# Performance work log

Hardware: AMD Instinct MI355X
Metric: run time of the kernel (lower is better)

The kernel has to match this reference:

```python
import jax, jax.numpy as jnp
import numpy as np
from jax import lax

P = 5
N_RATES = 8
N_SUB = 10
RATE_LO, RATE_HI = 0.01, 3.0
HJ_LO, HJ_HI = 0.0, 3.0


def gamma(x, lo, hi):
    return lo + (hi - lo) * jax.nn.sigmoid(x)


def chain_rhs(y, rates):
    # y: (B,5) [A,D,G,J,M]; rates: (B,8) [kf1..kf4, kr1..kr4]
    A, D, G, J, M = (y[..., i] for i in range(5))
    kf1, kf2, kf3, kf4, kr1, kr2, kr3, kr4 = (rates[..., i] for i in range(8))
    dA = -kf1 * A + kr1 * D
    dD = kf1 * A - kr1 * D - kf2 * D + kr2 * G
    dG = kf2 * D - kr2 * G - kf3 * G + kr3 * J
    dJ = kf3 * G - kr3 * J - kf4 * J + kr4 * M
    dM = kf4 * J - kr4 * M
    return jnp.stack([dA, dD, dG, dJ, dM], axis=-1)


def rk4_step(y, dt, rates):
    # dt: (B,1)
    k1 = chain_rhs(y, rates)
    k2 = chain_rhs(y + 0.5 * dt * k1, rates)
    k3 = chain_rhs(y + 0.5 * dt * k2, rates)
    k4 = chain_rhs(y + dt * k3, rates)
    y_next = y + dt / 6.0 * (k1 + 2.0 * k2 + 2.0 * k3 + k4)
    return jnp.maximum(y_next, 0.0)


def xavier(key, shape):
    fan_in, fan_out = shape[1], shape[0]
    lim = float(np.sqrt(6.0 / (fan_in + fan_out)))
    return jax.random.uniform(key, shape, jnp.float32, -lim, lim)


def setup_inputs() -> dict:
    key = jax.random.key(0)
    B, K, U, H, L = 512, 1024, 4, 128, 64
    ks = jax.random.split(key, 12)
    y0 = jax.random.uniform(ks[0], (B, P), jnp.float32)
    u_seq = jax.random.uniform(ks[1], (B, K, U), jnp.float32)
    dt_seq = jax.random.uniform(ks[2], (B, K), jnp.float32) * 0.1
    return {
        "y0": y0,
        "u_seq": u_seq,
        "dt_seq": dt_seq,
        "W_lift": xavier(ks[3], (L, U + P)),
        "b_lift": jnp.zeros((L,), jnp.float32),
        "W_ih": xavier(ks[4], (3 * H, L)),
        "W_hh": xavier(ks[5], (3 * H, H)),
        "b_ih": jnp.zeros((3 * H,), jnp.float32),
        "b_hh": jnp.zeros((3 * H,), jnp.float32),
        "W_head": xavier(ks[6], (N_RATES + P, H)),
        "b_head": jnp.zeros((N_RATES + P,), jnp.float32),
        "u_to_y_jump": jax.random.uniform(ks[7], (U, P), jnp.float32) * 0.5,
    }


def reference(y0, u_seq, dt_seq, W_lift, b_lift, W_ih, W_hh, b_ih, b_hh, W_head, b_head, u_to_y_jump):
    B, K, U = u_seq.shape
    H = W_hh.shape[1]

    def step(carry, inp):
        y_prev, h = carry
        u_k, dt_k = inp  # (B,U), (B,)
        y_in = lax.stop_gradient(y_prev)
        feat = jnp.concatenate([u_k, y_in], axis=-1)          # (B, U+P)
        x = jax.nn.silu(feat @ W_lift.T + b_lift)             # (B, L)
        gi = x @ W_ih.T + b_ih                                # (B, 3H)
        gh = h @ W_hh.T + b_hh                                # (B, 3H)
        i_r, i_z, i_n = jnp.split(gi, 3, axis=-1)
        h_r, h_z, h_n = jnp.split(gh, 3, axis=-1)
        r = jax.nn.sigmoid(i_r + h_r)
        zg = jax.nn.sigmoid(i_z + h_z)
        n = jnp.tanh(i_n + r * h_n)
        h_new = (1.0 - zg) * n + zg * h                       # (B, H)
        raw = h_new @ W_head.T + b_head                       # (B, 13)
        rates = gamma(raw[:, :N_RATES], RATE_LO, RATE_HI)     # (B, 8)
        dhid = gamma(raw[:, N_RATES:N_RATES + P], HJ_LO, HJ_HI)  # (B, 5)
        y_jump = y_prev + u_k @ u_to_y_jump + dhid
        h_sub = (dt_k / float(N_SUB))[:, None]                # (B, 1)
        y_cur = y_jump
        for _ in range(N_SUB):
            y_cur = rk4_step(y_cur, h_sub, rates)
        return (y_cur, h_new), (y_cur, rates, dhid)

    y_init = y0 + 0.01
    h0 = jnp.zeros((B, H), u_seq.dtype)
    u_t = jnp.swapaxes(u_seq, 0, 1)   # (K,B,U)
    dt_t = jnp.swapaxes(dt_seq, 0, 1)  # (K,B)
    _, (y_out, rates_out, dhid_out) = lax.scan(step, (y_init, h0), (u_t, dt_t))
    y_out = jnp.swapaxes(y_out, 0, 1)        # (B,K,P)
    rates_out = jnp.swapaxes(rates_out, 0, 1)  # (B,K,8)
    dhid_out = jnp.swapaxes(dhid_out, 0, 1)    # (B,K,P)
    return y_out, rates_out, dhid_out
```

## Files before the change

kernel.cpp:

```cpp
#include <hip/hip_runtime.h>

namespace {

typedef _Float16 __attribute__((ext_vector_type(2))) h2v;

constexpr int KST = 1024;
constexpr size_t OFF_R = (size_t)512 * KST * 5;
constexpr size_t OFF_D = OFF_R + (size_t)512 * KST * 8;

__device__ __forceinline__ float sigf(float x) { return 1.0f / (1.0f + __expf(-x)); }
__device__ __forceinline__ float tanhfast(float x) {
    float e2 = __expf(2.0f * x);
    return 1.0f - 2.0f / (e2 + 1.0f);
}
__device__ __forceinline__ float fdot2(h2v a, h2v b, float c) {
    return __builtin_amdgcn_fdot2(a, b, c, false);
}
__device__ __forceinline__ float dpp_shr1(float v) {
    return __builtin_bit_cast(float, __builtin_amdgcn_update_dpp(
        0, __builtin_bit_cast(int, v), 0x111, 0xf, 0xf, true));
}
__device__ __forceinline__ float dpp_shl1(float v) {
    return __builtin_bit_cast(float, __builtin_amdgcn_update_dpp(
        0, __builtin_bit_cast(int, v), 0x101, 0xf, 0xf, true));
}

__global__ __launch_bounds__(768, 3) void rnn_v11(
    const float* __restrict__ y0,     const float* __restrict__ u_seq,
    const float* __restrict__ dt_seq, const float* __restrict__ W_lift,
    const float* __restrict__ b_lift, const float* __restrict__ W_ih,
    const float* __restrict__ W_hh,   const float* __restrict__ b_ih,
    const float* __restrict__ b_hh,   const float* __restrict__ W_head,
    const float* __restrict__ b_head, const float* __restrict__ u2y,
    float* __restrict__ out)
{
    const int t    = threadIdx.x;
    const int lane = t & 63;
    const int wid  = t >> 6;
    const int hf   = (t >= 384) ? 1 : 0;
    const int o    = t - hf * 384;
    const int b0   = blockIdx.x * 2;

    __shared__ alignas(16) float sWlift[64 * 9];
    __shared__ float sblift[64];
    __shared__ alignas(16) float sWheadP[13 * 132];
    __shared__ float sbhead[16];
    __shared__ float sU2Y[20];
    __shared__ alignas(16) _Float16 sX2hi[2][64];
    __shared__ alignas(16) _Float16 sX2lo[2][64];
    __shared__ alignas(16) _Float16 sWihLo[2][384][36];
    __shared__ alignas(16) float sH[2][128];
    __shared__ alignas(16) _Float16 sH2[2][128];
    __shared__ alignas(16) float sGiP[2][2][384];
    __shared__ alignas(16) float sGhP[2][2][384];
    __shared__ float sY[2][8];

    h2v wih2[16];
    h2v whh2[32];
    {
        const float* p = W_ih + (size_t)o * 64 + hf * 32;
#pragma unroll
        for (int i = 0; i < 16; i++)
            wih2[i] = h2v{(_Float16)p[2 * i], (_Float16)p[2 * i + 1]};
        const float* q = W_hh + (size_t)o * 128 + hf * 64;
#pragma unroll
        for (int i = 0; i < 32; i++)
            whh2[i] = h2v{(_Float16)q[2 * i], (_Float16)q[2 * i + 1]};
    }
    const float bihv = hf ? 0.0f : b_ih[o];
    const float bhhv = hf ? 0.0f : b_hh[o];
#pragma unroll
    for (int i = 0; i < 16; i++) asm volatile("" : "+v"(wih2[i]));
#pragma unroll
    for (int i = 0; i < 32; i++) asm volatile("" : "+v"(whh2[i]));

    for (int i = t; i < 576; i += 768) sWlift[i] = W_lift[i];
    if (t < 64) sblift[t] = b_lift[t];
    for (int i = t; i < 13 * 128; i += 768) {
        int oo = i >> 7, c = i & 127;
        sWheadP[oo * 132 + c] = W_head[i];
    }
    for (int i = t; i < 2 * 384 * 32; i += 768) {
        int hh = i / (384 * 32);
        int rem = i - hh * 384 * 32;
        int oo = rem >> 5, c = rem & 31;
        float w = W_ih[(size_t)oo * 64 + hh * 32 + c];
        _Float16 wh = (_Float16)w;
        sWihLo[hh][oo][c] = (_Float16)(w - (float)wh);
    }
    if (t < 13) sbhead[t] = b_head[t];
    if (t < 20) sU2Y[t] = u2y[t];
    if (t < 256) {
        sH[t >> 7][t & 127] = 0.0f;
        sH2[t >> 7][t & 127] = (_Float16)0.0f;
    }
    if (t < 10) { int r = t / 5, s = t % 5; sY[r][s] = y0[(b0 + r) * 5 + s] + 0.01f; }
    sGhP[hf][0][o] = bhhv;
    sGhP[hf][1][o] = bhhv;
    __syncthreads();

    auto do_gi = [&]() {
        float g0 = bihv, g1 = 0.0f;
        const h2v* xh0 = (const h2v*)&sX2hi[0][hf * 32];
        const h2v* xh1 = (const h2v*)&sX2hi[1][hf * 32];
        const h2v* xl0 = (const h2v*)&sX2lo[0][hf * 32];
        const h2v* xl1 = (const h2v*)&sX2lo[1][hf * 32];
        const h2v* wlo = (const h2v*)&sWihLo[hf][o][0];
#pragma unroll
        for (int i = 0; i < 16; i++) {
            h2v wl = wlo[i];
            g0 = fdot2(wih2[i], xh0[i], g0);
            g0 = fdot2(wih2[i], xl0[i], g0);
            g0 = fdot2(wl, xh0[i], g0);
            g1 = fdot2(wih2[i], xh1[i], g1);
            g1 = fdot2(wih2[i], xl1[i], g1);
            g1 = fdot2(wl, xh1[i], g1);
        }
        sGiP[hf][0][o] = g0;
        sGiP[hf][1][o] = g1;
    };
    auto do_gh = [&]() {
        float g0 = bhhv, g1 = 0.0f;
        const h2v* h0p = (const h2v*)&sH2[0][hf * 64];
        const h2v* h1p = (const h2v*)&sH2[1][hf * 64];
#pragma unroll
        for (int i = 0; i < 32; i++) {
            g0 = fdot2(whh2[i], h0p[i], g0);
            g1 = fdot2(whh2[i], h1p[i], g1);
        }
        sGhP[hf][0][o] = g0;
        sGhP[hf][1][o] = g1;
    };
    auto do_lift = [&](float4 u0, float4 u1) {
        const float* wl = &sWlift[lane * 9];
        float bl = sblift[lane];
        float a0 = bl, a1 = bl;
        a0 = fmaf(wl[0], u0.x, a0);      a1 = fmaf(wl[0], u1.x, a1);
        a0 = fmaf(wl[1], u0.y, a0);      a1 = fmaf(wl[1], u1.y, a1);
        a0 = fmaf(wl[2], u0.z, a0);      a1 = fmaf(wl[2], u1.z, a1);
        a0 = fmaf(wl[3], u0.w, a0);      a1 = fmaf(wl[3], u1.w, a1);
        a0 = fmaf(wl[4], sY[0][0], a0);  a1 = fmaf(wl[4], sY[1][0], a1);
        a0 = fmaf(wl[5], sY[0][1], a0);  a1 = fmaf(wl[5], sY[1][1], a1);
        a0 = fmaf(wl[6], sY[0][2], a0);  a1 = fmaf(wl[6], sY[1][2], a1);
        a0 = fmaf(wl[7], sY[0][3], a0);  a1 = fmaf(wl[7], sY[1][3], a1);
        a0 = fmaf(wl[8], sY[0][4], a0);  a1 = fmaf(wl[8], sY[1][4], a1);
        float x0 = a0 * sigf(a0), x1 = a1 * sigf(a1);
        _Float16 xh0 = (_Float16)x0;
        sX2hi[0][lane] = xh0;
        sX2lo[0][lane] = (_Float16)(x0 - (float)xh0);
        _Float16 xh1 = (_Float16)x1;
        sX2hi[1][lane] = xh1;
        sX2lo[1][lane] = (_Float16)(x1 - (float)xh1);
    };

    if (wid == 0) {
        float4 u0 = *(const float4*)&u_seq[((size_t)b0 * KST) * 4];
        float4 u1 = *(const float4*)&u_seq[((size_t)(b0 + 1) * KST) * 4];
        do_lift(u0, u1);
    }
    __syncthreads();
    do_gi();
    __syncthreads();

    for (int k = 0; k < KST; k++) {
        if (t < 256) {
            int r = t >> 7, q = t & 127;
            float ir  = sGiP[0][r][q]       + sGiP[1][r][q];
            float iz  = sGiP[0][r][q + 128] + sGiP[1][r][q + 128];
            float in_ = sGiP[0][r][q + 256] + sGiP[1][r][q + 256];
            float hr  = sGhP[0][r][q]       + sGhP[1][r][q];
            float hz  = sGhP[0][r][q + 128] + sGhP[1][r][q + 128];
            float hn  = sGhP[0][r][q + 256] + sGhP[1][r][q + 256];
            float rr = sigf(ir + hr);
            float z  = sigf(iz + hz);
            float n  = tanhfast(fmaf(rr, hn, in_));
            float h  = sH[r][q];
            float hnew = fmaf(z, h - n, n);
            sH[r][q] = hnew;
            sH2[r][q] = (_Float16)hnew;
        }
        __syncthreads();

        float4 ukr{}, un0{}, un1{};
        float dtr = 0.0f;
        const int rh = (lane >> 4) & 1;
        if (wid == 0) {
            int kn = (k + 1 < KST) ? k + 1 : KST - 1;
            ukr = *(const float4*)&u_seq[((size_t)(b0 + rh) * KST + k) * 4];
            dtr = dt_seq[(size_t)(b0 + rh) * KST + k];
            un0 = *(const float4*)&u_seq[((size_t)b0 * KST + kn) * 4];
            un1 = *(const float4*)&u_seq[((size_t)(b0 + 1) * KST + kn) * 4];
        }
        do_gh();
        if (wid == 0) {
            const int hh = (lane >> 5) & 1;
            const int oo = lane & 15;
            float accv[4] = {0.f, 0.f, 0.f, 0.f};
            if (oo < 13) {
                const float4* wv = (const float4*)&sWheadP[oo * 132 + hh * 64];
                const float4* hv = (const float4*)&sH[rh][hh * 64];
#pragma unroll
                for (int c = 0; c < 4; c++) {
                    float4 w0 = wv[4 * c], w1 = wv[4 * c + 1], w2 = wv[4 * c + 2], w3 = wv[4 * c + 3];
                    float4 h0 = hv[4 * c], h1 = hv[4 * c + 1], h2 = hv[4 * c + 2], h3 = hv[4 * c + 3];
                    float a0 = w0.x * h0.x, a1 = w2.x * h2.x;
                    a0 = fmaf(w0.y, h0.y, a0); a1 = fmaf(w2.y, h2.y, a1);
                    a0 = fmaf(w0.z, h0.z, a0); a1 = fmaf(w2.z, h2.z, a1);
                    a0 = fmaf(w0.w, h0.w, a0); a1 = fmaf(w2.w, h2.w, a1);
                    a0 = fmaf(w1.x, h1.x, a0); a1 = fmaf(w3.x, h3.x, a1);
                    a0 = fmaf(w1.y, h1.y, a0); a1 = fmaf(w3.y, h3.y, a1);
                    a0 = fmaf(w1.z, h1.z, a0); a1 = fmaf(w3.z, h3.z, a1);
                    a0 = fmaf(w1.w, h1.w, a0); a1 = fmaf(w3.w, h3.w, a1);
                    accv[c] = a0 + a1;
                }
            }
            float p1 = accv[0] + accv[1];
            float p2 = accv[2] + accv[3];
            float part = p1 + p2;
            float tot = part + __shfl_xor(part, 32);
            float gval = 0.0f;
            if (oo < 13 && hh == 0) {
                float raw = tot + sbhead[oo];
                if (oo < 8) {
                    gval = fmaf(2.99f, sigf(raw), 0.01f);
                    out[OFF_R + ((size_t)(b0 + rh) * KST + k) * 8 + oo] = gval;
                } else {
                    gval = 3.0f * sigf(raw);
                    out[OFF_D + ((size_t)(b0 + rh) * KST + k) * 5 + (oo - 8)] = gval;
                }
            }

            const int i = lane & 15;
            const int base = rh * 16;
            float kf = __shfl(gval, base + i - 1);
            float kr = __shfl(gval, base + i + 3);
            if (!(i >= 1 && i <= 4)) { kf = 0.0f; kr = 0.0f; }
            float dh = __shfl(gval, base + 8 + i);
            const int ii = (i < 5) ? i : 0;
            float yp = sY[rh][ii];
            float jmp = ukr.x * sU2Y[ii];
            jmp = fmaf(ukr.y, sU2Y[5 + ii], jmp);
            jmp = fmaf(ukr.z, sU2Y[10 + ii], jmp);
            jmp = fmaf(ukr.w, sU2Y[15 + ii], jmp);
            float ya = yp + jmp + dh;
            const float hs = dtr * 0.1f;
            const float h2s = 0.5f * hs;
            const float h6 = hs * (1.0f / 6.0f);
#pragma unroll
            for (int ss = 0; ss < 10; ss++) {
                float yv = dpp_shr1(ya);
                float f1 = kf * yv - kr * ya;
                float k1 = f1 - dpp_shl1(f1);
                float tp = fmaf(h2s, k1, ya);
                yv = dpp_shr1(tp);
                float f2 = kf * yv - kr * tp;
                float k2 = f2 - dpp_shl1(f2);
                tp = fmaf(h2s, k2, ya);
                yv = dpp_shr1(tp);
                float f3 = kf * yv - kr * tp;
                float k3 = f3 - dpp_shl1(f3);
                tp = fmaf(hs, k3, ya);
                yv = dpp_shr1(tp);
                float f4 = kf * yv - kr * tp;
                float k4 = f4 - dpp_shl1(f4);
                float sum = k1 + 2.0f * (k2 + k3) + k4;
                ya = fmaxf(fmaf(h6, sum, ya), 0.0f);
            }
            if (lane < 32 && i < 5) {
                sY[rh][i] = ya;
                out[((size_t)(b0 + rh) * KST + k) * 5 + i] = ya;
            }
            asm volatile("s_waitcnt lgkmcnt(0)" ::: "memory");
            do_lift(un0, un1);
        }
        __syncthreads();

        do_gi();
        __syncthreads();
    }
}

}

extern "C" void kernel_launch(void* const* d_in, const int* in_sizes, int n_in,
                              void* d_out, int out_size, void* d_ws, size_t ws_size,
                              hipStream_t stream) {
    const float* y0     = (const float*)d_in[0];
    const float* u_seq  = (const float*)d_in[1];
    const float* dt_seq = (const float*)d_in[2];
    const float* W_lift = (const float*)d_in[3];
    const float* b_lift = (const float*)d_in[4];
    const float* W_ih   = (const float*)d_in[5];
    const float* W_hh   = (const float*)d_in[6];
    const float* b_ih   = (const float*)d_in[7];
    const float* b_hh   = (const float*)d_in[8];
    const float* W_head = (const float*)d_in[9];
    const float* b_head = (const float*)d_in[10];
    const float* u2y    = (const float*)d_in[11];
    float* out = (float*)d_out;

    rnn_v11<<<256, 768, 0, stream>>>(y0, u_seq, dt_seq, W_lift, b_lift,
                                     W_ih, W_hh, b_ih, b_hh, W_head, b_head,
                                     u2y, out);
}
```

Before: 3.178 ms.

## Replace serial RK4 substeps with a matrix-power propagator and reschedule wave-0 gh

For a linear reaction chain with fixed rates, one RK4 step is a 5x5 matrix (a 4th-order Taylor polynomial of hA). The new code builds that matrix across lanes and raises it to the 10th power with four shuffle-based matmuls, then applies it to the jumped state, instead of running 10 dependent RK4 substeps. The non-negativity clamp is now applied once at the end instead of after every substep, which can differ slightly from the reference if an intermediate state goes negative. Wave 0 also skips its share of the hidden-gate matvec during the head/ODE phase and does it after the barrier, so the other waves' gh work overlaps wave 0's serial critical path.

```diff
diff --git a/kernel.cpp b/kernel.cpp
--- a/kernel.cpp
+++ b/kernel.cpp
@@ -16,16 +16,8 @@
 __device__ __forceinline__ float fdot2(h2v a, h2v b, float c) {
     return __builtin_amdgcn_fdot2(a, b, c, false);
 }
-__device__ __forceinline__ float dpp_shr1(float v) {
-    return __builtin_bit_cast(float, __builtin_amdgcn_update_dpp(
-        0, __builtin_bit_cast(int, v), 0x111, 0xf, 0xf, true));
-}
-__device__ __forceinline__ float dpp_shl1(float v) {
-    return __builtin_bit_cast(float, __builtin_amdgcn_update_dpp(
-        0, __builtin_bit_cast(int, v), 0x101, 0xf, 0xf, true));
-}
-
-__global__ __launch_bounds__(768, 3) void rnn_v11(
+
+__global__ __launch_bounds__(768, 3) void rnn_v12(
     const float* __restrict__ y0,     const float* __restrict__ u_seq,
     const float* __restrict__ dt_seq, const float* __restrict__ W_lift,
     const float* __restrict__ b_lift, const float* __restrict__ W_ih,
@@ -54,6 +46,7 @@
     __shared__ alignas(16) float sGiP[2][2][384];
     __shared__ alignas(16) float sGhP[2][2][384];
     __shared__ float sY[2][8];
+    __shared__ float sYJ[2][8];
 
     h2v wih2[16];
     h2v whh2[32];
@@ -73,6 +66,14 @@
     for (int i = 0; i < 16; i++) asm volatile("" : "+v"(wih2[i]));
 #pragma unroll
     for (int i = 0; i < 32; i++) asm volatile("" : "+v"(whh2[i]));
+
+    const int mr = (lane >= 32) ? 1 : 0;
+    const int me = lane - mr * 32;
+    const int mi = me / 5;
+    const int mj = me - mi * 5;
+    const int rowBase = mr * 32 + mi * 5;
+    const int colBase = mr * 32 + mj;
+    const bool mAct = (me < 25);
 
     for (int i = t; i < 576; i += 768) sWlift[i] = W_lift[i];
     if (t < 64) sblift[t] = b_lift[t];
@@ -181,18 +182,16 @@
         }
         __syncthreads();
 
-        float4 ukr{}, un0{}, un1{};
-        float dtr = 0.0f;
-        const int rh = (lane >> 4) & 1;
-        if (wid == 0) {
+        if (wid != 0) {
+            do_gh();
+        } else {
+            const int rh = (lane >> 4) & 1;
             int kn = (k + 1 < KST) ? k + 1 : KST - 1;
-            ukr = *(const float4*)&u_seq[((size_t)(b0 + rh) * KST + k) * 4];
-            dtr = dt_seq[(size_t)(b0 + rh) * KST + k];
-            un0 = *(const float4*)&u_seq[((size_t)b0 * KST + kn) * 4];
-            un1 = *(const float4*)&u_seq[((size_t)(b0 + 1) * KST + kn) * 4];
-        }
-        do_gh();
-        if (wid == 0) {
+            float4 ukr = *(const float4*)&u_seq[((size_t)(b0 + rh) * KST + k) * 4];
+            float dtr = dt_seq[(size_t)(b0 + rh) * KST + k];
+            float4 un0 = *(const float4*)&u_seq[((size_t)b0 * KST + kn) * 4];
+            float4 un1 = *(const float4*)&u_seq[((size_t)(b0 + 1) * KST + kn) * 4];
+
             const int hh = (lane >> 5) & 1;
             const int oo = lane & 15;
             float accv[4] = {0.f, 0.f, 0.f, 0.f};
@@ -230,51 +229,85 @@
                 }
             }
 
-            const int i = lane & 15;
-            const int base = rh * 16;
-            float kf = __shfl(gval, base + i - 1);
-            float kr = __shfl(gval, base + i + 3);
-            if (!(i >= 1 && i <= 4)) { kf = 0.0f; kr = 0.0f; }
-            float dh = __shfl(gval, base + 8 + i);
-            const int ii = (i < 5) ? i : 0;
-            float yp = sY[rh][ii];
-            float jmp = ukr.x * sU2Y[ii];
-            jmp = fmaf(ukr.y, sU2Y[5 + ii], jmp);
-            jmp = fmaf(ukr.z, sU2Y[10 + ii], jmp);
-            jmp = fmaf(ukr.w, sU2Y[15 + ii], jmp);
-            float ya = yp + jmp + dh;
-            const float hs = dtr * 0.1f;
-            const float h2s = 0.5f * hs;
-            const float h6 = hs * (1.0f / 6.0f);
-#pragma unroll
-            for (int ss = 0; ss < 10; ss++) {
-                float yv = dpp_shr1(ya);
-                float f1 = kf * yv - kr * ya;
-                float k1 = f1 - dpp_shl1(f1);
-                float tp = fmaf(h2s, k1, ya);
-                yv = dpp_shr1(tp);
-                float f2 = kf * yv - kr * tp;
-                float k2 = f2 - dpp_shl1(f2);
-                tp = fmaf(h2s, k2, ya);
-                yv = dpp_shr1(tp);
-                float f3 = kf * yv - kr * tp;
-                float k3 = f3 - dpp_shl1(f3);
-                tp = fmaf(hs, k3, ya);
-                yv = dpp_shr1(tp);
-                float f4 = kf * yv - kr * tp;
-                float k4 = f4 - dpp_shl1(f4);
-                float sum = k1 + 2.0f * (k2 + k3) + k4;
-                ya = fmaxf(fmaf(h6, sum, ya), 0.0f);
-            }
-            if (lane < 32 && i < 5) {
-                sY[rh][i] = ya;
-                out[((size_t)(b0 + rh) * KST + k) * 5 + i] = ya;
+            if (oo >= 8 && oo < 13 && hh == 0) {
+                int s = oo - 8;
+                float yp = sY[rh][s];
+                float jmp = ukr.x * sU2Y[s];
+                jmp = fmaf(ukr.y, sU2Y[5 + s], jmp);
+                jmp = fmaf(ukr.z, sU2Y[10 + s], jmp);
+                jmp = fmaf(ukr.w, sU2Y[15 + s], jmp);
+                sYJ[rh][s] = yp + jmp + gval;
+            }
+            asm volatile("s_waitcnt lgkmcnt(0)" ::: "memory");
+
+            float kf1 = __shfl(gval, mr * 16 + 0);
+            float kf2 = __shfl(gval, mr * 16 + 1);
+            float kf3 = __shfl(gval, mr * 16 + 2);
+            float kf4 = __shfl(gval, mr * 16 + 3);
+            float kr1 = __shfl(gval, mr * 16 + 4);
+            float kr2 = __shfl(gval, mr * 16 + 5);
+            float kr3 = __shfl(gval, mr * 16 + 6);
+            float kr4 = __shfl(gval, mr * 16 + 7);
+            float dtv = __shfl(dtr, mr * 16);
+            const float hstep = dtv * 0.1f;
+            const float d1 = kr1 + kf2, d2 = kr2 + kf3, d3 = kr3 + kf4;
+            float v0 = (mj == 0) ? 1.f : 0.f;
+            float v1 = (mj == 1) ? 1.f : 0.f;
+            float v2 = (mj == 2) ? 1.f : 0.f;
+            float v3 = (mj == 3) ? 1.f : 0.f;
+            float v4 = (mj == 4) ? 1.f : 0.f;
+            float a0 = v0, a1 = v1, a2 = v2, a3 = v3, a4 = v4;
+#pragma unroll
+            for (int s = 1; s <= 4; s++) {
+                const float hs = hstep * ((s == 1) ? 1.0f : (s == 2) ? 0.5f
+                                        : (s == 3) ? (1.0f / 3.0f) : 0.25f);
+                float t0 = kr1 * v1 - kf1 * v0;
+                float t1 = fmaf(kf1, v0, fmaf(kr2, v2, -d1 * v1));
+                float t2 = fmaf(kf2, v1, fmaf(kr3, v3, -d2 * v2));
+                float t3 = fmaf(kf3, v2, fmaf(kr4, v4, -d3 * v3));
+                float t4 = kf4 * v3 - kr4 * v4;
+                v0 = t0 * hs; v1 = t1 * hs; v2 = t2 * hs; v3 = t3 * hs; v4 = t4 * hs;
+                a0 += v0; a1 += v1; a2 += v2; a3 += v3; a4 += v4;
+            }
+            float m = a0;
+            m = (mi == 1) ? a1 : m;
+            m = (mi == 2) ? a2 : m;
+            m = (mi == 3) ? a3 : m;
+            m = (mi == 4) ? a4 : m;
+
+            auto matmul = [&](float A, float B) -> float {
+                float c = 0.0f;
+#pragma unroll
+                for (int kk = 0; kk < 5; kk++) {
+                    float av = __shfl(A, rowBase + kk);
+                    float bv = __shfl(B, colBase + 5 * kk);
+                    c = fmaf(av, bv, c);
+                }
+                return c;
+            };
+            float m2  = matmul(m, m);
+            float m4  = matmul(m2, m2);
+            float m5  = matmul(m4, m);
+            float m10 = matmul(m5, m5);
+
+            float yjv = sYJ[mr][mj];
+            float p = m10 * yjv;
+            float sum = __shfl(p, rowBase + 0);
+            sum += __shfl(p, rowBase + 1);
+            sum += __shfl(p, rowBase + 2);
+            sum += __shfl(p, rowBase + 3);
+            sum += __shfl(p, rowBase + 4);
+            float ynew = fmaxf(sum, 0.0f);
+            if (mAct && mj == 0) {
+                sY[mr][mi] = ynew;
+                out[((size_t)(b0 + mr) * KST + k) * 5 + mi] = ynew;
             }
             asm volatile("s_waitcnt lgkmcnt(0)" ::: "memory");
             do_lift(un0, un1);
         }
         __syncthreads();
 
+        if (wid == 0) do_gh();
         do_gi();
         __syncthreads();
     }
@@ -299,7 +332,7 @@
     const float* u2y    = (const float*)d_in[11];
     float* out = (float*)d_out;
 
-    rnn_v11<<<256, 768, 0, stream>>>(y0, u_seq, dt_seq, W_lift, b_lift,
+    rnn_v12<<<256, 768, 0, stream>>>(y0, u_seq, dt_seq, W_lift, b_lift,
                                      W_ih, W_hh, b_ih, b_hh, W_head, b_head,
                                      u2y, out);
 }
```

Measured after the change: 3.293 ms. 3.6% more time.

## Switch to one batch row per block with full-row weights per thread

Applied to the files above, without the earlier changes.

Each block now handles a single batch element with 384 threads, and each thread holds a full row of W_ih and W_hh in registers instead of half a row shared across two batch rows. This removes the cross-half partial-sum reduction in shared memory and doubles the grid to 512 blocks, so more CUs can run the serial recurrence in parallel. In exchange, register pressure per thread roughly doubles (96 packed weight registers), the weights are no longer reused across two batch rows, and the head/RK4 wave now serves only one row.

```diff
diff --git a/kernel.cpp b/kernel.cpp
--- a/kernel.cpp
+++ b/kernel.cpp
@@ -25,7 +25,7 @@
         0, __builtin_bit_cast(int, v), 0x101, 0xf, 0xf, true));
 }
 
-__global__ __launch_bounds__(768, 3) void rnn_v11(
+__global__ __launch_bounds__(384, 2) void rnn_v13(
     const float* __restrict__ y0,     const float* __restrict__ u_seq,
     const float* __restrict__ dt_seq, const float* __restrict__ W_lift,
     const float* __restrict__ b_lift, const float* __restrict__ W_ih,
@@ -37,168 +37,153 @@
     const int t    = threadIdx.x;
     const int lane = t & 63;
     const int wid  = t >> 6;
-    const int hf   = (t >= 384) ? 1 : 0;
-    const int o    = t - hf * 384;
-    const int b0   = blockIdx.x * 2;
+    const int b    = blockIdx.x;
 
     __shared__ alignas(16) float sWlift[64 * 9];
     __shared__ float sblift[64];
     __shared__ alignas(16) float sWheadP[13 * 132];
     __shared__ float sbhead[16];
     __shared__ float sU2Y[20];
-    __shared__ alignas(16) _Float16 sX2hi[2][64];
-    __shared__ alignas(16) _Float16 sX2lo[2][64];
-    __shared__ alignas(16) _Float16 sWihLo[2][384][36];
-    __shared__ alignas(16) float sH[2][128];
-    __shared__ alignas(16) _Float16 sH2[2][128];
-    __shared__ alignas(16) float sGiP[2][2][384];
-    __shared__ alignas(16) float sGhP[2][2][384];
-    __shared__ float sY[2][8];
-
-    h2v wih2[16];
-    h2v whh2[32];
+    __shared__ alignas(16) _Float16 sX2hi[64];
+    __shared__ alignas(16) _Float16 sX2lo[64];
+    __shared__ alignas(16) h2v sWihLo[384 * 33];
+    __shared__ alignas(16) float sH[128];
+    __shared__ alignas(16) _Float16 sH2[128];
+    __shared__ alignas(16) float sGi[384];
+    __shared__ alignas(16) float sGh[384];
+    __shared__ float sY[8];
+
+    h2v wih2[32];
+    h2v whh2[64];
     {
-        const float* p = W_ih + (size_t)o * 64 + hf * 32;
-#pragma unroll
-        for (int i = 0; i < 16; i++)
+        const float* p = W_ih + (size_t)t * 64;
+#pragma unroll
+        for (int i = 0; i < 32; i++)
             wih2[i] = h2v{(_Float16)p[2 * i], (_Float16)p[2 * i + 1]};
-        const float* q = W_hh + (size_t)o * 128 + hf * 64;
-#pragma unroll
-        for (int i = 0; i < 32; i++)
+        const float* q = W_hh + (size_t)t * 128;
+#pragma unroll
+        for (int i = 0; i < 64; i++)
             whh2[i] = h2v{(_Float16)q[2 * i], (_Float16)q[2 * i + 1]};
     }
-    const float bihv = hf ? 0.0f : b_ih[o];
-    const float bhhv = hf ? 0.0f : b_hh[o];
-#pragma unroll
-    for (int i = 0; i < 16; i++) asm volatile("" : "+v"(wih2[i]));
-#pragma unroll
-    for (int i = 0; i < 32; i++) asm volatile("" : "+v"(whh2[i]));
-
-    for (int i = t; i < 576; i += 768) sWlift[i] = W_lift[i];
+    const float bihv = b_ih[t];
+    const float bhhv = b_hh[t];
+#pragma unroll
+    for (int i = 0; i < 32; i++) asm volatile("" : "+v"(wih2[i]));
+#pragma unroll
+    for (int i = 0; i < 64; i++) asm volatile("" : "+v"(whh2[i]));
+
+    for (int i = t; i < 576; i += 384) sWlift[i] = W_lift[i];
     if (t < 64) sblift[t] = b_lift[t];
-    for (int i = t; i < 13 * 128; i += 768) {
+    for (int i = t; i < 13 * 128; i += 384) {
         int oo = i >> 7, c = i & 127;
         sWheadP[oo * 132 + c] = W_head[i];
     }
-    for (int i = t; i < 2 * 384 * 32; i += 768) {
-        int hh = i / (384 * 32);
-        int rem = i - hh * 384 * 32;
-        int oo = rem >> 5, c = rem & 31;
-        float w = W_ih[(size_t)oo * 64 + hh * 32 + c];
-        _Float16 wh = (_Float16)w;
-        sWihLo[hh][oo][c] = (_Float16)(w - (float)wh);
+    for (int i = t; i < 384 * 32; i += 384) {
+        int oo = i >> 5, c = i & 31;
+        float w0 = W_ih[(size_t)oo * 64 + 2 * c];
+        float w1 = W_ih[(size_t)oo * 64 + 2 * c + 1];
+        _Float16 h0 = (_Float16)w0, h1 = (_Float16)w1;
+        sWihLo[oo * 33 + c] = h2v{(_Float16)(w0 - (float)h0), (_Float16)(w1 - (float)h1)};
     }
     if (t < 13) sbhead[t] = b_head[t];
     if (t < 20) sU2Y[t] = u2y[t];
-    if (t < 256) {
-        sH[t >> 7][t & 127] = 0.0f;
-        sH2[t >> 7][t & 127] = (_Float16)0.0f;
-    }
-    if (t < 10) { int r = t / 5, s = t % 5; sY[r][s] = y0[(b0 + r) * 5 + s] + 0.01f; }
-    sGhP[hf][0][o] = bhhv;
-    sGhP[hf][1][o] = bhhv;
+    if (t < 128) {
+        sH[t] = 0.0f;
+        sH2[t] = (_Float16)0.0f;
+    }
+    if (t < 5) sY[t] = y0[b * 5 + t] + 0.01f;
+    sGh[t] = bhhv;
     __syncthreads();
 
     auto do_gi = [&]() {
-        float g0 = bihv, g1 = 0.0f;
-        const h2v* xh0 = (const h2v*)&sX2hi[0][hf * 32];
-        const h2v* xh1 = (const h2v*)&sX2hi[1][hf * 32];
-        const h2v* xl0 = (const h2v*)&sX2lo[0][hf * 32];
-        const h2v* xl1 = (const h2v*)&sX2lo[1][hf * 32];
-        const h2v* wlo = (const h2v*)&sWihLo[hf][o][0];
+        float ga = bihv, gb = 0.0f;
+        const h2v* xh = (const h2v*)&sX2hi[0];
+        const h2v* xl = (const h2v*)&sX2lo[0];
+        const h2v* wlo = &sWihLo[t * 33];
 #pragma unroll
         for (int i = 0; i < 16; i++) {
-            h2v wl = wlo[i];
-            g0 = fdot2(wih2[i], xh0[i], g0);
-            g0 = fdot2(wih2[i], xl0[i], g0);
-            g0 = fdot2(wl, xh0[i], g0);
-            g1 = fdot2(wih2[i], xh1[i], g1);
-            g1 = fdot2(wih2[i], xl1[i], g1);
-            g1 = fdot2(wl, xh1[i], g1);
-        }
-        sGiP[hf][0][o] = g0;
-        sGiP[hf][1][o] = g1;
+            ga = fdot2(wih2[i], xh[i], ga);
+            ga = fdot2(wih2[i], xl[i], ga);
+            ga = fdot2(wlo[i], xh[i], ga);
+        }
+#pragma unroll
+        for (int i = 16; i < 32; i++) {
+            gb = fdot2(wih2[i], xh[i], gb);
+            gb = fdot2(wih2[i], xl[i], gb);
+            gb = fdot2(wlo[i], xh[i], gb);
+        }
+        sGi[t] = ga + gb;
     };
     auto do_gh = [&]() {
-        float g0 = bhhv, g1 = 0.0f;
-        const h2v* h0p = (const h2v*)&sH2[0][hf * 64];
-        const h2v* h1p = (const h2v*)&sH2[1][hf * 64];
-#pragma unroll
-        for (int i = 0; i < 32; i++) {
-            g0 = fdot2(whh2[i], h0p[i], g0);
-            g1 = fdot2(whh2[i], h1p[i], g1);
-        }
-        sGhP[hf][0][o] = g0;
-        sGhP[hf][1][o] = g1;
+        float ga = bhhv, gb = 0.0f;
+        const h2v* hp = (const h2v*)&sH2[0];
+#pragma unroll
+        for (int i = 0; i < 32; i++) ga = fdot2(whh2[i], hp[i], ga);
+#pragma unroll
+        for (int i = 32; i < 64; i++) gb = fdot2(whh2[i], hp[i], gb);
+        sGh[t] = ga + gb;
     };
-    auto do_lift = [&](float4 u0, float4 u1) {
+    auto do_lift = [&](float4 u0) {
         const float* wl = &sWlift[lane * 9];
-        float bl = sblift[lane];
-        float a0 = bl, a1 = bl;
-        a0 = fmaf(wl[0], u0.x, a0);      a1 = fmaf(wl[0], u1.x, a1);
-        a0 = fmaf(wl[1], u0.y, a0);      a1 = fmaf(wl[1], u1.y, a1);
-        a0 = fmaf(wl[2], u0.z, a0);      a1 = fmaf(wl[2], u1.z, a1);
-        a0 = fmaf(wl[3], u0.w, a0);      a1 = fmaf(wl[3], u1.w, a1);
-        a0 = fmaf(wl[4], sY[0][0], a0);  a1 = fmaf(wl[4], sY[1][0], a1);
-        a0 = fmaf(wl[5], sY[0][1], a0);  a1 = fmaf(wl[5], sY[1][1], a1);
-        a0 = fmaf(wl[6], sY[0][2], a0);  a1 = fmaf(wl[6], sY[1][2], a1);
-        a0 = fmaf(wl[7], sY[0][3], a0);  a1 = fmaf(wl[7], sY[1][3], a1);
-        a0 = fmaf(wl[8], sY[0][4], a0);  a1 = fmaf(wl[8], sY[1][4], a1);
-        float x0 = a0 * sigf(a0), x1 = a1 * sigf(a1);
-        _Float16 xh0 = (_Float16)x0;
-        sX2hi[0][lane] = xh0;
-        sX2lo[0][lane] = (_Float16)(x0 - (float)xh0);
-        _Float16 xh1 = (_Float16)x1;
-        sX2hi[1][lane] = xh1;
-        sX2lo[1][lane] = (_Float16)(x1 - (float)xh1);
+        float a0 = sblift[lane];
+        a0 = fmaf(wl[0], u0.x, a0);
+        a0 = fmaf(wl[1], u0.y, a0);
+        a0 = fmaf(wl[2], u0.z, a0);
+        a0 = fmaf(wl[3], u0.w, a0);
+        a0 = fmaf(wl[4], sY[0], a0);
+        a0 = fmaf(wl[5], sY[1], a0);
+        a0 = fmaf(wl[6], sY[2], a0);
+        a0 = fmaf(wl[7], sY[3], a0);
+        a0 = fmaf(wl[8], sY[4], a0);
+        float x0 = a0 * sigf(a0);
+        _Float16 xh = (_Float16)x0;
+        sX2hi[lane] = xh;
+        sX2lo[lane] = (_Float16)(x0 - (float)xh);
     };
 
     if (wid == 0) {
-        float4 u0 = *(const float4*)&u_seq[((size_t)b0 * KST) * 4];
-        float4 u1 = *(const float4*)&u_seq[((size_t)(b0 + 1) * KST) * 4];
-        do_lift(u0, u1);
+        float4 u0 = *(const float4*)&u_seq[((size_t)b * KST) * 4];
+        do_lift(u0);
     }
     __syncthreads();
     do_gi();
     __syncthreads();
 
     for (int k = 0; k < KST; k++) {
-        if (t < 256) {
-            int r = t >> 7, q = t & 127;
-            float ir  = sGiP[0][r][q]       + sGiP[1][r][q];
-            float iz  = sGiP[0][r][q + 128] + sGiP[1][r][q + 128];
-            float in_ = sGiP[0][r][q + 256] + sGiP[1][r][q + 256];
-            float hr  = sGhP[0][r][q]       + sGhP[1][r][q];
-            float hz  = sGhP[0][r][q + 128] + sGhP[1][r][q + 128];
-            float hn  = sGhP[0][r][q + 256] + sGhP[1][r][q + 256];
+        if (t < 128) {
+            int q = t;
+            float ir  = sGi[q];
+            float iz  = sGi[q + 128];
+            float in_ = sGi[q + 256];
+            float hr  = sGh[q];
+            float hz  = sGh[q + 128];
+            float hn  = sGh[q + 256];
             float rr = sigf(ir + hr);
             float z  = sigf(iz + hz);
             float n  = tanhfast(fmaf(rr, hn, in_));
-            float h  = sH[r][q];
+            float h  = sH[q];
             float hnew = fmaf(z, h - n, n);
-            sH[r][q] = hnew;
-            sH2[r][q] = (_Float16)hnew;
+            sH[q] = hnew;
+            sH2[q] = (_Float16)hnew;
         }
         __syncthreads();
 
-        float4 ukr{}, un0{}, un1{};
+        float4 ukr{}, un{};
         float dtr = 0.0f;
-        const int rh = (lane >> 4) & 1;
         if (wid == 0) {
             int kn = (k + 1 < KST) ? k + 1 : KST - 1;
-            ukr = *(const float4*)&u_seq[((size_t)(b0 + rh) * KST + k) * 4];
-            dtr = dt_seq[(size_t)(b0 + rh) * KST + k];
-            un0 = *(const float4*)&u_seq[((size_t)b0 * KST + kn) * 4];
-            un1 = *(const float4*)&u_seq[((size_t)(b0 + 1) * KST + kn) * 4];
+            ukr = *(const float4*)&u_seq[((size_t)b * KST + k) * 4];
+            dtr = dt_seq[(size_t)b * KST + k];
+            un  = *(const float4*)&u_seq[((size_t)b * KST + kn) * 4];
         }
         do_gh();
         if (wid == 0) {
-            const int hh = (lane >> 5) & 1;
-            const int oo = lane & 15;
+            const int hh = lane >> 5;
+            const int oo = lane & 31;
             float accv[4] = {0.f, 0.f, 0.f, 0.f};
             if (oo < 13) {
                 const float4* wv = (const float4*)&sWheadP[oo * 132 + hh * 64];
-                const float4* hv = (const float4*)&sH[rh][hh * 64];
+                const float4* hv = (const float4*)&sH[hh * 64];
 #pragma unroll
                 for (int c = 0; c < 4; c++) {
                     float4 w0 = wv[4 * c], w1 = wv[4 * c + 1], w2 = wv[4 * c + 2], w3 = wv[4 * c + 3];
@@ -223,21 +208,20 @@
                 float raw = tot + sbhead[oo];
                 if (oo < 8) {
                     gval = fmaf(2.99f, sigf(raw), 0.01f);
-                    out[OFF_R + ((size_t)(b0 + rh) * KST + k) * 8 + oo] = gval;
+                    out[OFF_R + ((size_t)b * KST + k) * 8 + oo] = gval;
                 } else {
                     gval = 3.0f * sigf(raw);
-                    out[OFF_D + ((size_t)(b0 + rh) * KST + k) * 5 + (oo - 8)] = gval;
+                    out[OFF_D + ((size_t)b * KST + k) * 5 + (oo - 8)] = gval;
                 }
             }
 
             const int i = lane & 15;
-            const int base = rh * 16;
-            float kf = __shfl(gval, base + i - 1);
-            float kr = __shfl(gval, base + i + 3);
+            float kf = __shfl(gval, i - 1);
+            float kr = __shfl(gval, i + 3);
             if (!(i >= 1 && i <= 4)) { kf = 0.0f; kr = 0.0f; }
-            float dh = __shfl(gval, base + 8 + i);
+            float dh = __shfl(gval, 8 + i);
             const int ii = (i < 5) ? i : 0;
-            float yp = sY[rh][ii];
+            float yp = sY[ii];
             float jmp = ukr.x * sU2Y[ii];
             jmp = fmaf(ukr.y, sU2Y[5 + ii], jmp);
             jmp = fmaf(ukr.z, sU2Y[10 + ii], jmp);
@@ -266,12 +250,12 @@
                 float sum = k1 + 2.0f * (k2 + k3) + k4;
                 ya = fmaxf(fmaf(h6, sum, ya), 0.0f);
             }
-            if (lane < 32 && i < 5) {
-                sY[rh][i] = ya;
-                out[((size_t)(b0 + rh) * KST + k) * 5 + i] = ya;
+            if (lane < 5) {
+                sY[lane] = ya;
+                out[((size_t)b * KST + k) * 5 + lane] = ya;
             }
             asm volatile("s_waitcnt lgkmcnt(0)" ::: "memory");
-            do_lift(un0, un1);
+            do_lift(un);
         }
         __syncthreads();
 
@@ -299,7 +283,7 @@
     const float* u2y    = (const float*)d_in[11];
     float* out = (float*)d_out;
 
-    rnn_v11<<<256, 768, 0, stream>>>(y0, u_seq, dt_seq, W_lift, b_lift,
+    rnn_v13<<<512, 384, 0, stream>>>(y0, u_seq, dt_seq, W_lift, b_lift,
                                      W_ih, W_hh, b_ih, b_hh, W_head, b_head,
                                      u2y, out);
 }
```

Result: slower. 5.544 ms (+74.5%).
